# Performance work log

Measured on AMD Instinct MI355X. Metric: run time of the kernel, lower is better.

The kernel has to match this reference:

```python
import jax, jax.numpy as jnp
import numpy as np

VOCAB = 64
H = 64
B = 128
L = 2048


def setup_inputs() -> dict:
    key = jax.random.key(0)
    ks = jax.random.split(key, 14)
    s = 0.02
    return {
        "x": jax.random.randint(ks[0], (B, L), 0, VOCAB),
        "embed": jax.random.normal(ks[1], (VOCAB, H), jnp.float32) * s,
        "w1": jax.random.normal(ks[2], (2 * H, H), jnp.float32) * s,
        "b1": jnp.zeros((2 * H,), jnp.float32),
        "w2": jax.random.normal(ks[3], (H, 2 * H), jnp.float32) * s,
        "b2": jnp.zeros((H,), jnp.float32),
        "ln_g": jnp.ones((H,), jnp.float32),
        "ln_b": jnp.zeros((H,), jnp.float32),
        "Wk": jax.random.normal(ks[4], (H, H), jnp.float32) * s,
        "Wv": jax.random.normal(ks[5], (H, H), jnp.float32) * s,
        "Wq": jax.random.normal(ks[6], (H, H), jnp.float32) * s,
        "Wout": jax.random.normal(ks[7], (VOCAB, H), jnp.float32) * s,
        "bout": jnp.zeros((VOCAB,), jnp.float32),
    }


def _encoder(x, embed, w1, b1, w2, b2, ln_g, ln_b):
    h0 = embed[x]  # [B,L,H]
    ff = jnp.maximum(h0 @ w1.T + b1, 0.0) @ w2.T + b2
    z = h0 + ff
    mu = z.mean(-1, keepdims=True)
    var = ((z - mu) ** 2).mean(-1, keepdims=True)
    return (z - mu) * jax.lax.rsqrt(var + 1e-5) * ln_g + ln_b


def reference(x, embed, w1, b1, w2, b2, ln_g, ln_b, Wk, Wv, Wq, Wout, bout):
    h = _encoder(x, embed, w1, b1, w2, b2, ln_g, ln_b)  # [B,L,H]
    K = h @ Wk.T
    K = K / jnp.maximum(jnp.linalg.norm(K, axis=-1, keepdims=True), 1e-12)  # F.normalize
    V = h @ Wv.T
    b, l, hd = h.shape

    def step(M, kv):
        k, v = kv  # [B,H], [B,H]
        pred = jnp.einsum('bij,bj->bi', M, k)  # M @ k
        M = M + (v - pred)[:, :, None] * k[:, None, :]  # delta-rule outer update
        return M, None

    M0 = jnp.zeros((b, hd, hd), h.dtype)
    M, _ = jax.lax.scan(step, M0, (K.transpose(1, 0, 2), V.transpose(1, 0, 2)))

    q = h[:, -1] @ Wq.T  # [B,H]
    slots = M.transpose(0, 2, 1)  # M^T per batch: [B,H,H]
    scores = jnp.einsum('bij,bj->bi', slots, q) / jnp.sqrt(jnp.asarray(hd, h.dtype))
    attn = jax.nn.softmax(scores, axis=-1)  # [B,H]
    ctx = jnp.einsum('bi,bij->bj', attn, slots)  # [B,H]
    return jnp.maximum(ctx, 0.0) @ Wout.T + bout  # [B,VOCAB]
```

## Files before the change

### kernel.cpp

```cpp
#include <hip/hip_runtime.h>
#include <hip/hip_bf16.h>

#define VOCAB 64
#define H 64
#define NB 128
#define SL 2048

__global__ __launch_bounds__(64) void k_tables(
    const float* __restrict__ embed, const float* __restrict__ w1, const float* __restrict__ b1,
    const float* __restrict__ w2, const float* __restrict__ b2,
    const float* __restrict__ ln_g, const float* __restrict__ ln_b,
    const float* __restrict__ Wk, const float* __restrict__ Wv, const float* __restrict__ Wq,
    float* __restrict__ Ktab, float* __restrict__ Vtab, float* __restrict__ qtab)
{
  const int t = blockIdx.x;
  const int i = threadIdx.x;
  __shared__ float h0s[H];
  __shared__ float ff1s[2 * H];
  __shared__ float hs[H];

  h0s[i] = embed[t * H + i];
  __syncthreads();

  const float4* w1v = (const float4*)w1;
  float a0 = b1[i], a1 = b1[i + H];
#pragma unroll
  for (int j4 = 0; j4 < 16; ++j4) {
    const float4 hv = *(const float4*)&h0s[j4 * 4];
    const float4 wa = w1v[i * 16 + j4];
    const float4 wb = w1v[(i + H) * 16 + j4];
    a0 = fmaf(wa.x, hv.x, fmaf(wa.y, hv.y, fmaf(wa.z, hv.z, fmaf(wa.w, hv.w, a0))));
    a1 = fmaf(wb.x, hv.x, fmaf(wb.y, hv.y, fmaf(wb.z, hv.z, fmaf(wb.w, hv.w, a1))));
  }
  ff1s[i] = fmaxf(a0, 0.f);
  ff1s[i + H] = fmaxf(a1, 0.f);
  __syncthreads();

  const float4* w2v = (const float4*)w2;
  float z = h0s[i] + b2[i];
#pragma unroll
  for (int o4 = 0; o4 < 32; ++o4) {
    const float4 fv = *(const float4*)&ff1s[o4 * 4];
    const float4 wv = w2v[i * 32 + o4];
    z = fmaf(wv.x, fv.x, fmaf(wv.y, fv.y, fmaf(wv.z, fv.z, fmaf(wv.w, fv.w, z))));
  }

  float s = z;
#pragma unroll
  for (int m = 1; m < 64; m <<= 1) s += __shfl_xor(s, m);
  const float mu = s * (1.f / 64.f);
  const float d = z - mu;
  float s2 = d * d;
#pragma unroll
  for (int m = 1; m < 64; m <<= 1) s2 += __shfl_xor(s2, m);
  const float var = s2 * (1.f / 64.f);
  const float hv2 = d * rsqrtf(var + 1e-5f) * ln_g[i] + ln_b[i];
  hs[i] = hv2;
  __syncthreads();

  const float4* wkv = (const float4*)Wk;
  const float4* wvv = (const float4*)Wv;
  const float4* wqv = (const float4*)Wq;
  float kk = 0.f, vv = 0.f, qq = 0.f;
#pragma unroll
  for (int j4 = 0; j4 < 16; ++j4) {
    const float4 hj = *(const float4*)&hs[j4 * 4];
    const float4 ak = wkv[i * 16 + j4];
    const float4 av = wvv[i * 16 + j4];
    const float4 aq = wqv[i * 16 + j4];
    kk = fmaf(ak.x, hj.x, fmaf(ak.y, hj.y, fmaf(ak.z, hj.z, fmaf(ak.w, hj.w, kk))));
    vv = fmaf(av.x, hj.x, fmaf(av.y, hj.y, fmaf(av.z, hj.z, fmaf(av.w, hj.w, vv))));
    qq = fmaf(aq.x, hj.x, fmaf(aq.y, hj.y, fmaf(aq.z, hj.z, fmaf(aq.w, hj.w, qq))));
  }
  float n2 = kk * kk;
#pragma unroll
  for (int m = 1; m < 64; m <<= 1) n2 += __shfl_xor(n2, m);
  const float inv = 1.f / fmaxf(sqrtf(n2), 1e-12f);
  Ktab[t * H + i] = kk * inv;
  Vtab[t * H + i] = vv;
  qtab[t * H + i] = qq;
}

__device__ __forceinline__ int rfl(int v) { return __builtin_amdgcn_readfirstlane(v); }
__device__ __forceinline__ float rdl(float v, int sl) {
  return __int_as_float(__builtin_amdgcn_readlane(__float_as_int(v), sl));
}

__global__ __launch_bounds__(256) void k_scan(
    const int* __restrict__ x, const float* __restrict__ Ktab, const float* __restrict__ Vtab,
    float* __restrict__ Mout)
{
  const int bb = blockIdx.x >> 1;
  const int half = blockIdx.x & 1;
  const int tid = threadIdx.x;
  const int lane = tid & 63;
  const int wave = tid >> 6;
  const int r0 = wave * 8;

  __shared__ float smem[16456];
  float* Gs  = smem;
  float* Ks  = smem + 4096;
  float* KTs = smem + 8192;
  float* Vs  = smem + 12352;
  int*   xsh = (int*)(smem + 14400);

#pragma unroll
  for (int u = 0; u < 4; ++u) {
    const int f4i = u * 256 + tid;
    const float4 kv = ((const float4*)Ktab)[f4i];
    ((float4*)Ks)[f4i] = kv;
    const int row = f4i >> 4, c4 = (f4i & 15) * 4;
    KTs[(c4 + 0) * 65 + row] = kv.x;
    KTs[(c4 + 1) * 65 + row] = kv.y;
    KTs[(c4 + 2) * 65 + row] = kv.z;
    KTs[(c4 + 3) * 65 + row] = kv.w;
  }
  {
    const int t = tid >> 2, rq = (tid & 3) * 8;
    const float4 v0 = *(const float4*)&Vtab[t * H + half * 32 + rq];
    const float4 v1 = *(const float4*)&Vtab[t * H + half * 32 + rq + 4];
    *(float4*)&Vs[t * 32 + rq] = v0;
    *(float4*)&Vs[t * 32 + rq + 4] = v1;
  }
  {
    const int4* gx4 = (const int4*)(x + bb * SL);
    ((int4*)xsh)[tid] = gx4[tid];
    ((int4*)xsh)[256 + tid] = gx4[256 + tid];
    if (tid < 2) ((int4*)xsh)[512 + tid] = make_int4(0, 0, 0, 0);
  }
  __syncthreads();

  {
    const int abase = wave * 16;
#pragma unroll 1
    for (int ar = 0; ar < 16; ++ar) {
      const int a = abase + ar;
      float acc = 0.f;
#pragma unroll
      for (int i = 0; i < H; i += 4) {
        const float4 ka = *(const float4*)&Ks[a * 64 + i];
        acc = fmaf(ka.x, KTs[(i + 0) * 65 + lane], acc);
        acc = fmaf(ka.y, KTs[(i + 1) * 65 + lane], acc);
        acc = fmaf(ka.z, KTs[(i + 2) * 65 + lane], acc);
        acc = fmaf(ka.w, KTs[(i + 3) * 65 + lane], acc);
      }
      Gs[a * 64 + lane] = acc;
    }
  }
  __syncthreads();

  float P[8], Mr[8];
#pragma unroll
  for (int j = 0; j < 8; ++j) { P[j] = 0.f; Mr[j] = 0.f; }

#define PREF(G_, K_, V0_, V1_, a_)                       \
  {                                                      \
    G_  = Gs[(a_) * 64 + lane];                          \
    K_  = Ks[(a_) * 64 + lane];                          \
    V0_ = *(const float4*)&Vs[(a_) * 32 + r0];           \
    V1_ = *(const float4*)&Vs[(a_) * 32 + r0 + 4];       \
  }

#define STEP(G_, K_, V0_, V1_, sa_)                      \
  {                                                      \
    const float d0 = V0_.x - rdl(P[0], sa_);             \
    const float d1 = V0_.y - rdl(P[1], sa_);             \
    const float d2 = V0_.z - rdl(P[2], sa_);             \
    const float d3 = V0_.w - rdl(P[3], sa_);             \
    const float d4 = V1_.x - rdl(P[4], sa_);             \
    const float d5 = V1_.y - rdl(P[5], sa_);             \
    const float d6 = V1_.z - rdl(P[6], sa_);             \
    const float d7 = V1_.w - rdl(P[7], sa_);             \
    P[0] = fmaf(d0, G_, P[0]);  Mr[0] = fmaf(d0, K_, Mr[0]); \
    P[1] = fmaf(d1, G_, P[1]);  Mr[1] = fmaf(d1, K_, Mr[1]); \
    P[2] = fmaf(d2, G_, P[2]);  Mr[2] = fmaf(d2, K_, Mr[2]); \
    P[3] = fmaf(d3, G_, P[3]);  Mr[3] = fmaf(d3, K_, Mr[3]); \
    P[4] = fmaf(d4, G_, P[4]);  Mr[4] = fmaf(d4, K_, Mr[4]); \
    P[5] = fmaf(d5, G_, P[5]);  Mr[5] = fmaf(d5, K_, Mr[5]); \
    P[6] = fmaf(d6, G_, P[6]);  Mr[6] = fmaf(d6, K_, Mr[6]); \
    P[7] = fmaf(d7, G_, P[7]);  Mr[7] = fmaf(d7, K_, Mr[7]); \
  }

  float gA, kA, gB, kB, gC, kC, gD, kD;
  float4 vA0, vA1, vB0, vB1, vC0, vC1, vD0, vD1;

  int4 tg = ((const int4*)xsh)[0];
  int s0 = rfl(tg.x);
  int s1 = rfl(tg.y);
  PREF(gA, kA, vA0, vA1, s0);
  PREF(gB, kB, vB0, vB1, s1);

#pragma unroll 1
  for (int n = 0; n < SL / 4; ++n) {
    const int4 tgN = ((const int4*)xsh)[n + 1];
    const int s2 = rfl(tg.z);
    PREF(gC, kC, vC0, vC1, s2);
    STEP(gA, kA, vA0, vA1, s0);
    const int s3 = rfl(tg.w);
    PREF(gD, kD, vD0, vD1, s3);
    STEP(gB, kB, vB0, vB1, s1);
    const int t0 = rfl(tgN.x);
    PREF(gA, kA, vA0, vA1, t0);
    STEP(gC, kC, vC0, vC1, s2);
    const int t1 = rfl(tgN.y);
    PREF(gB, kB, vB0, vB1, t1);
    STEP(gD, kD, vD0, vD1, s3);
    tg = tgN; s0 = t0; s1 = t1;
  }
#undef PREF
#undef STEP

  float* mp = Mout + ((size_t)bb * H + half * 32 + r0) * H + lane;
#pragma unroll
  for (int j = 0; j < 8; ++j) mp[j * H] = Mr[j];
}

__global__ __launch_bounds__(64) void k_final(
    const int* __restrict__ x, const float* __restrict__ Mws, const float* __restrict__ qtab,
    const float* __restrict__ Wout, const float* __restrict__ bout, float* __restrict__ out)
{
  const int b = blockIdx.x;
  const int i = threadIdx.x;
  __shared__ float Ml[H * 65];
  __shared__ float qs[H];
  __shared__ float attns[H];
  __shared__ float rcs[H];

  const float* Mg = Mws + (size_t)b * H * H;
#pragma unroll
  for (int j4 = 0; j4 < H; j4 += 4) {
    const float4 v = *(const float4*)(Mg + i * H + j4);
    Ml[i * 65 + j4 + 0] = v.x;
    Ml[i * 65 + j4 + 1] = v.y;
    Ml[i * 65 + j4 + 2] = v.z;
    Ml[i * 65 + j4 + 3] = v.w;
  }
  const int tok = x[b * SL + (SL - 1)];
  qs[i] = qtab[tok * H + i];
  __syncthreads();

  float acc = 0.f;
#pragma unroll
  for (int j = 0; j < H; ++j) acc = fmaf(Ml[j * 65 + i], qs[j], acc);
  const float sc = acc * 0.125f;

  float mx = sc;
#pragma unroll
  for (int m = 1; m < 64; m <<= 1) mx = fmaxf(mx, __shfl_xor(mx, m));
  const float e = expf(sc - mx);
  float ssum = e;
#pragma unroll
  for (int m = 1; m < 64; m <<= 1) ssum += __shfl_xor(ssum, m);
  attns[i] = e / ssum;
  __syncthreads();

  float cx = 0.f;
#pragma unroll
  for (int jj = 0; jj < H; ++jj) cx = fmaf(attns[jj], Ml[i * 65 + jj], cx);
  rcs[i] = fmaxf(cx, 0.f);
  __syncthreads();

  float o = bout[i];
#pragma unroll
  for (int j = 0; j < H; ++j) o = fmaf(Wout[i * H + j], rcs[j], o);
  out[b * VOCAB + i] = o;
}

extern "C" void kernel_launch(void* const* d_in, const int* in_sizes, int n_in,
                              void* d_out, int out_size, void* d_ws, size_t ws_size,
                              hipStream_t stream) {
  const int*   x     = (const int*)d_in[0];
  const float* embed = (const float*)d_in[1];
  const float* w1    = (const float*)d_in[2];
  const float* b1    = (const float*)d_in[3];
  const float* w2    = (const float*)d_in[4];
  const float* b2    = (const float*)d_in[5];
  const float* ln_g  = (const float*)d_in[6];
  const float* ln_b  = (const float*)d_in[7];
  const float* Wk    = (const float*)d_in[8];
  const float* Wv    = (const float*)d_in[9];
  const float* Wq    = (const float*)d_in[10];
  const float* Wout  = (const float*)d_in[11];
  const float* bout  = (const float*)d_in[12];

  float* ws   = (float*)d_ws;
  float* Ktab = ws;
  float* Vtab = ws + 4096;
  float* qtab = ws + 8192;
  float* Mws  = ws + 12288;

  k_tables<<<dim3(VOCAB), dim3(H), 0, stream>>>(embed, w1, b1, w2, b2, ln_g, ln_b,
                                                Wk, Wv, Wq, Ktab, Vtab, qtab);
  k_scan<<<dim3(2 * NB), dim3(256), 0, stream>>>(x, Ktab, Vtab, Mws);
  k_final<<<dim3(NB), dim3(64), 0, stream>>>(x, Mws, qtab, Wout, bout, (float*)d_out);
}
```

Baseline: 245.1 us.

## Split delta-rule scan across eight waves with four rows each and interleave G/K

The scan kernel now uses 512 threads (8 waves), each owning 4 rows of the memory matrix instead of 8, which halves the per-step serial dependency chain per wave. The Gram and K tables are interleaved into one float2 array so each step fetches G and K with a single LDS load. The trade-offs are more waves per block and more LDS traffic on the V and token loads, and the block's shared memory grows.

```diff
diff --git a/kernel.cpp b/kernel.cpp
--- a/kernel.cpp
+++ b/kernel.cpp
@@ -86,7 +86,7 @@
   return __int_as_float(__builtin_amdgcn_readlane(__float_as_int(v), sl));
 }
 
-__global__ __launch_bounds__(256) void k_scan(
+__global__ __launch_bounds__(512) void k_scan(
     const int* __restrict__ x, const float* __restrict__ Ktab, const float* __restrict__ Vtab,
     float* __restrict__ Mout)
 {
@@ -95,18 +95,18 @@
   const int tid = threadIdx.x;
   const int lane = tid & 63;
   const int wave = tid >> 6;
-  const int r0 = wave * 8;
-
-  __shared__ float smem[16456];
-  float* Gs  = smem;
-  float* Ks  = smem + 4096;
-  float* KTs = smem + 8192;
-  float* Vs  = smem + 12352;
-  int*   xsh = (int*)(smem + 14400);
-
-#pragma unroll
-  for (int u = 0; u < 4; ++u) {
-    const int f4i = u * 256 + tid;
+  const int r0 = wave * 4;
+
+  __shared__ float smem[20552];
+  float* Ks  = smem;
+  float* KTs = smem + 4096;
+  float* GKs = smem + 8256;
+  float* Vs  = smem + 16448;
+  int*   xsh = (int*)(smem + 18496);
+
+#pragma unroll
+  for (int u = 0; u < 2; ++u) {
+    const int f4i = u * 512 + tid;
     const float4 kv = ((const float4*)Ktab)[f4i];
     ((float4*)Ks)[f4i] = kv;
     const int row = f4i >> 4, c4 = (f4i & 15) * 4;
@@ -115,25 +115,26 @@
     KTs[(c4 + 2) * 65 + row] = kv.z;
     KTs[(c4 + 3) * 65 + row] = kv.w;
   }
+#pragma unroll
+  for (int u = 0; u < 8; ++u) {
+    const int idx = u * 512 + tid;
+    GKs[idx * 2 + 1] = Ktab[idx];
+  }
   {
-    const int t = tid >> 2, rq = (tid & 3) * 8;
-    const float4 v0 = *(const float4*)&Vtab[t * H + half * 32 + rq];
-    const float4 v1 = *(const float4*)&Vtab[t * H + half * 32 + rq + 4];
-    *(float4*)&Vs[t * 32 + rq] = v0;
-    *(float4*)&Vs[t * 32 + rq + 4] = v1;
+    const int t = tid >> 3, rq = (tid & 7) * 4;
+    *(float4*)&Vs[t * 32 + rq] = *(const float4*)&Vtab[t * H + half * 32 + rq];
   }
   {
     const int4* gx4 = (const int4*)(x + bb * SL);
     ((int4*)xsh)[tid] = gx4[tid];
-    ((int4*)xsh)[256 + tid] = gx4[256 + tid];
     if (tid < 2) ((int4*)xsh)[512 + tid] = make_int4(0, 0, 0, 0);
   }
   __syncthreads();
 
   {
-    const int abase = wave * 16;
+    const int abase = wave * 8;
 #pragma unroll 1
-    for (int ar = 0; ar < 16; ++ar) {
+    for (int ar = 0; ar < 8; ++ar) {
       const int a = abase + ar;
       float acc = 0.f;
 #pragma unroll
@@ -144,67 +145,58 @@
         acc = fmaf(ka.z, KTs[(i + 2) * 65 + lane], acc);
         acc = fmaf(ka.w, KTs[(i + 3) * 65 + lane], acc);
       }
-      Gs[a * 64 + lane] = acc;
+      GKs[(a * 64 + lane) * 2] = acc;
     }
   }
   __syncthreads();
 
-  float P[8], Mr[8];
-#pragma unroll
-  for (int j = 0; j < 8; ++j) { P[j] = 0.f; Mr[j] = 0.f; }
-
-#define PREF(G_, K_, V0_, V1_, a_)                       \
-  {                                                      \
-    G_  = Gs[(a_) * 64 + lane];                          \
-    K_  = Ks[(a_) * 64 + lane];                          \
-    V0_ = *(const float4*)&Vs[(a_) * 32 + r0];           \
-    V1_ = *(const float4*)&Vs[(a_) * 32 + r0 + 4];       \
-  }
-
-#define STEP(G_, K_, V0_, V1_, sa_)                      \
-  {                                                      \
-    const float d0 = V0_.x - rdl(P[0], sa_);             \
-    const float d1 = V0_.y - rdl(P[1], sa_);             \
-    const float d2 = V0_.z - rdl(P[2], sa_);             \
-    const float d3 = V0_.w - rdl(P[3], sa_);             \
-    const float d4 = V1_.x - rdl(P[4], sa_);             \
-    const float d5 = V1_.y - rdl(P[5], sa_);             \
-    const float d6 = V1_.z - rdl(P[6], sa_);             \
-    const float d7 = V1_.w - rdl(P[7], sa_);             \
+  float P[4], Mr[4];
+#pragma unroll
+  for (int j = 0; j < 4; ++j) { P[j] = 0.f; Mr[j] = 0.f; }
+
+#define PREF(G_, K_, V_, a_)                              \
+  {                                                       \
+    const float2 gk = *(const float2*)&GKs[(a_) * 128 + lane * 2]; \
+    G_ = gk.x; K_ = gk.y;                                 \
+    V_ = *(const float4*)&Vs[(a_) * 32 + r0];             \
+  }
+
+#define STEP(G_, K_, V_, sa_)                             \
+  {                                                       \
+    const float d0 = V_.x - rdl(P[0], sa_);               \
+    const float d1 = V_.y - rdl(P[1], sa_);               \
+    const float d2 = V_.z - rdl(P[2], sa_);               \
+    const float d3 = V_.w - rdl(P[3], sa_);               \
     P[0] = fmaf(d0, G_, P[0]);  Mr[0] = fmaf(d0, K_, Mr[0]); \
     P[1] = fmaf(d1, G_, P[1]);  Mr[1] = fmaf(d1, K_, Mr[1]); \
     P[2] = fmaf(d2, G_, P[2]);  Mr[2] = fmaf(d2, K_, Mr[2]); \
     P[3] = fmaf(d3, G_, P[3]);  Mr[3] = fmaf(d3, K_, Mr[3]); \
-    P[4] = fmaf(d4, G_, P[4]);  Mr[4] = fmaf(d4, K_, Mr[4]); \
-    P[5] = fmaf(d5, G_, P[5]);  Mr[5] = fmaf(d5, K_, Mr[5]); \
-    P[6] = fmaf(d6, G_, P[6]);  Mr[6] = fmaf(d6, K_, Mr[6]); \
-    P[7] = fmaf(d7, G_, P[7]);  Mr[7] = fmaf(d7, K_, Mr[7]); \
   }
 
   float gA, kA, gB, kB, gC, kC, gD, kD;
-  float4 vA0, vA1, vB0, vB1, vC0, vC1, vD0, vD1;
+  float4 vA, vB, vC, vD;
 
   int4 tg = ((const int4*)xsh)[0];
   int s0 = rfl(tg.x);
   int s1 = rfl(tg.y);
-  PREF(gA, kA, vA0, vA1, s0);
-  PREF(gB, kB, vB0, vB1, s1);
+  PREF(gA, kA, vA, s0);
+  PREF(gB, kB, vB, s1);
 
 #pragma unroll 1
   for (int n = 0; n < SL / 4; ++n) {
     const int4 tgN = ((const int4*)xsh)[n + 1];
     const int s2 = rfl(tg.z);
-    PREF(gC, kC, vC0, vC1, s2);
-    STEP(gA, kA, vA0, vA1, s0);
+    PREF(gC, kC, vC, s2);
+    STEP(gA, kA, vA, s0);
     const int s3 = rfl(tg.w);
-    PREF(gD, kD, vD0, vD1, s3);
-    STEP(gB, kB, vB0, vB1, s1);
+    PREF(gD, kD, vD, s3);
+    STEP(gB, kB, vB, s1);
     const int t0 = rfl(tgN.x);
-    PREF(gA, kA, vA0, vA1, t0);
-    STEP(gC, kC, vC0, vC1, s2);
+    PREF(gA, kA, vA, t0);
+    STEP(gC, kC, vC, s2);
     const int t1 = rfl(tgN.y);
-    PREF(gB, kB, vB0, vB1, t1);
-    STEP(gD, kD, vD0, vD1, s3);
+    PREF(gB, kB, vB, t1);
+    STEP(gD, kD, vD, s3);
     tg = tgN; s0 = t0; s1 = t1;
   }
 #undef PREF
@@ -212,7 +204,7 @@
 
   float* mp = Mout + ((size_t)bb * H + half * 32 + r0) * H + lane;
 #pragma unroll
-  for (int j = 0; j < 8; ++j) mp[j * H] = Mr[j];
+  for (int j = 0; j < 4; ++j) mp[j * H] = Mr[j];
 }
 
 __global__ __launch_bounds__(64) void k_final(
@@ -291,6 +283,6 @@
 
   k_tables<<<dim3(VOCAB), dim3(H), 0, stream>>>(embed, w1, b1, w2, b2, ln_g, ln_b,
                                                 Wk, Wv, Wq, Ktab, Vtab, qtab);
-  k_scan<<<dim3(2 * NB), dim3(256), 0, stream>>>(x, Ktab, Vtab, Mws);
+  k_scan<<<dim3(2 * NB), dim3(512), 0, stream>>>(x, Ktab, Vtab, Mws);
   k_final<<<dim3(NB), dim3(64), 0, stream>>>(x, Mws, qtab, Wout, bout, (float*)d_out);
 }
```

After: 241.5 us. No clear change (-1.5%).
